# Kernel optimization log

Measured on AMD Instinct MI355X. Metric: run time of the kernel, lower is better.

The kernel has to match this reference:

```python
import jax, jax.numpy as jnp
import numpy as np

B, C, H, W = 8, 256, 64, 64
IC = 64  # inter_channels


def conv1x1(x, w, b):
    # x: [B,C,H,W], w: [O,C], b: [O]
    return jnp.einsum('bchw,oc->bohw', x, w) + b[None, :, None, None]


def maxpool2(x):
    # 2x2 max pool, stride 2. x: [B,C,H,W]
    b, c, h, w = x.shape
    return x.reshape(b, c, h // 2, 2, w // 2, 2).max(axis=(3, 5))


def setup_inputs() -> dict:
    key = jax.random.key(0)
    ks = jax.random.split(key, 9)
    s_in = 1.0 / np.sqrt(C)
    s_ic = 1.0 / np.sqrt(IC)
    return {
        'x': jax.random.normal(ks[0], (B, C, H, W), dtype=jnp.float32),
        'g_w': jax.random.uniform(ks[1], (IC, C), jnp.float32, -s_in, s_in),
        'g_b': jax.random.uniform(ks[2], (IC,), jnp.float32, -s_in, s_in),
        'theta_w': jax.random.uniform(ks[3], (IC, C), jnp.float32, -s_in, s_in),
        'theta_b': jax.random.uniform(ks[4], (IC,), jnp.float32, -s_in, s_in),
        'phi_w': jax.random.uniform(ks[5], (IC, C), jnp.float32, -s_in, s_in),
        'phi_b': jax.random.uniform(ks[6], (IC,), jnp.float32, -s_in, s_in),
        'W_w': jax.random.uniform(ks[7], (C, IC), jnp.float32, -np.sqrt(6.0 / IC), np.sqrt(6.0 / IC)),
        'W_b': jax.random.uniform(ks[8], (C,), jnp.float32, -s_ic, s_ic),
    }


def reference(x, g_w, g_b, theta_w, theta_b, phi_w, phi_b, W_w, W_b):
    b, c, h, w = x.shape
    n = h * w                     # query positions
    m = (h // 2) * (w // 2)       # pooled key/value positions

    v = maxpool2(conv1x1(x, g_w, g_b)).reshape(b, IC, m).transpose(0, 2, 1)   # [b,m,ic]
    q = conv1x1(x, theta_w, theta_b).reshape(b, IC, n).transpose(0, 2, 1)     # [b,n,ic]
    k = maxpool2(conv1x1(x, phi_w, phi_b)).reshape(b, IC, m)                  # [b,ic,m]

    attn = jax.nn.softmax(jnp.einsum('bni,bim->bnm', q, k), axis=-1)          # [b,n,m]
    attended = jnp.einsum('bnm,bmi->bni', attn, v)                            # [b,n,ic]
    attended = attended.transpose(0, 2, 1).reshape(b, IC, h, w)
    # F.interpolate to (h,w) is identity here: attended already has spatial (h,w)
    return conv1x1(attended, W_w, W_b) + x
```

## Files before the change

kernel.cpp:

```cpp
#include <hip/hip_runtime.h>

typedef unsigned short ushort_t;
typedef unsigned int   uint_t;

typedef __attribute__((ext_vector_type(8))) short  short8;
typedef __attribute__((ext_vector_type(4))) short  short4v;
typedef __attribute__((ext_vector_type(4))) float  float4v;

#define BB    8
#define CC    256
#define HH    64
#define WW2   64
#define NPIX  4096
#define MPOS  1024
#define ICH   64

__device__ __forceinline__ float bf2f(ushort_t u) {
  return __uint_as_float(((uint_t)u) << 16);
}
__device__ __forceinline__ ushort_t f2bf(float f) {
  uint_t i = __float_as_uint(f);
  uint_t r = (i + 0x7FFFu + ((i >> 16) & 1u)) >> 16;
  return (ushort_t)r;
}
__device__ __forceinline__ ushort_t f2bf_rna(float f) {
  return (ushort_t)((__float_as_uint(f) + 0x8000u) >> 16);
}
__device__ __forceinline__ uint_t pack2(float a, float b) {
  return (uint_t)f2bf(a) | ((uint_t)f2bf(b) << 16);
}

__device__ __forceinline__ void gl2lds16(const ushort_t* g, ushort_t* l) {
  __builtin_amdgcn_global_load_lds(
      (const __attribute__((address_space(1))) void*)g,
      (__attribute__((address_space(3))) void*)l, 16, 0, 0);
}

__global__ __launch_bounds__(256) void prep_kernel(
    const float* __restrict__ theta_w, const float* __restrict__ phi_w,
    const float* __restrict__ g_w, const float* __restrict__ W_w,
    const float* __restrict__ theta_b, const float* __restrict__ phi_b,
    const float* __restrict__ g_b,
    ushort_t* __restrict__ wA2, ushort_t* __restrict__ Wbf2,
    float* __restrict__ biasAll) {
  int i = blockIdx.x * 256 + threadIdx.x;
  if (i < 49152) {
    float v = (i < 16384) ? theta_w[i]
            : (i < 32768) ? phi_w[i - 16384]
                          : g_w[i - 32768];
    int o = i >> 8, c = i & 255;
    wA2[(c >> 3) * 1536 + o * 8 + (c & 7)] = f2bf(v);
  } else if (i < 65536) {
    int j = i - 49152;
    int o = j >> 6, ic = j & 63;
    Wbf2[(ic >> 3) * 2048 + o * 8 + (ic & 7)] = f2bf(W_w[j]);
  } else if (i < 65600)    biasAll[i - 65536] = theta_b[i - 65536];
  else if (i < 65664)      biasAll[i - 65536] = phi_b[i - 65600];
  else if (i < 65728)      biasAll[i - 65536] = g_b[i - 65664];
}

__global__ __launch_bounds__(256, 2) void qkv_kernel(
    const float* __restrict__ x, const ushort_t* __restrict__ wA2,
    const float* __restrict__ biasAll,
    ushort_t* __restrict__ qbuf, ushort_t* __restrict__ kTbuf,
    ushort_t* __restrict__ vTbuf) {
  __shared__ __align__(16) ushort_t Bsu[64 * 256];
  uint4* Bs16 = (uint4*)Bsu;
  int tid = threadIdx.x;
  int wave = tid >> 6, lane = tid & 63;
  int quad = lane >> 4, col = lane & 15;
  int b = blockIdx.x & 7, t = blockIdx.x >> 3;
  int rj = t >> 1, h = t & 1;

  {
    int pg = tid & 15, cb = tid >> 4;
    int prow = pg >> 3;
    int pcol = (pg * 4) & 31;
    const float* xsrc = x + (size_t)b * (CC * NPIX) +
                        (size_t)(2 * rj + prow) * WW2 + h * 32 + pcol;
    float4 v[16];
#pragma unroll
    for (int c = 0; c < 16; ++c)
      v[c] = *(const float4*)&xsrc[(size_t)(cb * 16 + c) * NPIX];
#pragma unroll
    for (int j = 0; j < 4; ++j) {
      int pos = pg * 4 + j;
      uint4 w0, w1;
      w0.x = pack2(v[0][j],  v[1][j]);
      w0.y = pack2(v[2][j],  v[3][j]);
      w0.z = pack2(v[4][j],  v[5][j]);
      w0.w = pack2(v[6][j],  v[7][j]);
      w1.x = pack2(v[8][j],  v[9][j]);
      w1.y = pack2(v[10][j], v[11][j]);
      w1.z = pack2(v[12][j], v[13][j]);
      w1.w = pack2(v[14][j], v[15][j]);
      int jb0 = cb * 2, jb1 = cb * 2 + 1;
      Bs16[pos * 32 + (jb0 & ~7) + ((jb0 & 7) ^ (pos & 7))] = w0;
      Bs16[pos * 32 + (jb1 & ~7) + ((jb1 & 7) ^ (pos & 7))] = w1;
    }
  }
  __syncthreads();

  float4v acc[3][4];
#pragma unroll
  for (int ot = 0; ot < 3; ++ot) {
    int ob = wave * 48 + ot * 16 + quad * 4;
    float4v bv;
#pragma unroll
    for (int r = 0; r < 4; ++r) bv[r] = biasAll[ob + r];
#pragma unroll
    for (int s = 0; s < 4; ++s) acc[ot][s] = bv;
  }

  const uint4* wA16 = (const uint4*)wA2;
#pragma unroll
  for (int ks = 0; ks < 8; ++ks) {
    int kblk = ks * 4 + quad;
    short8 aw[3];
#pragma unroll
    for (int ot = 0; ot < 3; ++ot) {
      uint4 a = wA16[kblk * 192 + wave * 48 + ot * 16 + col];
      aw[ot] = *(const short8*)&a;
    }
#pragma unroll
    for (int s = 0; s < 4; ++s) {
      int lp = s * 16 + col;
      uint4 braw = Bs16[lp * 32 + (kblk & ~7) + ((kblk & 7) ^ (lp & 7))];
      short8 bx = *(const short8*)&braw;
#pragma unroll
      for (int ot = 0; ot < 3; ++ot)
        acc[ot][s] = __builtin_amdgcn_mfma_f32_16x16x32_bf16(aw[ot], bx, acc[ot][s], 0, 0, 0);
    }
  }

#pragma unroll
  for (int ot = 0; ot < 3; ++ot) {
    int ob = wave * 48 + ot * 16;
    if (ob < 64) {
#pragma unroll
      for (int s = 0; s < 4; ++s) {
        int n = (2 * rj + (s >> 1)) * WW2 + h * 32 + (s & 1) * 16 + col;
        uint2 u;
        u.x = pack2(acc[ot][s][0], acc[ot][s][1]);
        u.y = pack2(acc[ot][s][2], acc[ot][s][3]);
        *(uint2*)&qbuf[((size_t)(b * NPIX + n)) * ICH + ob + quad * 4] = u;
      }
    } else if (ob < 128) {
#pragma unroll
      for (int s = 0; s < 2; ++s) {
        float4v pm;
#pragma unroll
        for (int r = 0; r < 4; ++r) {
          float v = fmaxf(acc[ot][s][r], acc[ot][s + 2][r]);
          pm[r] = fmaxf(v, __shfl_xor(v, 1));
        }
        if ((lane & 1) == 0) {
          int m = rj * 32 + h * 16 + s * 8 + (col >> 1);
          uint2 u;
          u.x = pack2(pm[0], pm[1]);
          u.y = pack2(pm[2], pm[3]);
          *(uint2*)&kTbuf[((size_t)(b * MPOS + m)) * ICH + (ob - 64) + quad * 4] = u;
        }
      }
    } else {
#pragma unroll
      for (int s = 0; s < 2; ++s) {
        float4v pm;
#pragma unroll
        for (int r = 0; r < 4; ++r) {
          float v = fmaxf(acc[ot][s][r], acc[ot][s + 2][r]);
          pm[r] = fmaxf(v, __shfl_xor(v, 1));
        }
        if ((lane & 1) == 0) {
          int m = rj * 32 + h * 16 + s * 8 + (col >> 1);
#pragma unroll
          for (int r = 0; r < 4; ++r)
            vTbuf[((size_t)(b * ICH + (ob - 128) + quad * 4 + r)) * MPOS + m] = f2bf(pm[r]);
        }
      }
    }
  }
}

__global__ __launch_bounds__(256, 2) void attn_out_kernel(
    const ushort_t* __restrict__ qbuf, const ushort_t* __restrict__ kTbuf,
    const ushort_t* __restrict__ vTbuf, const ushort_t* __restrict__ Wbf2,
    const float* __restrict__ W_b, const float* __restrict__ x,
    float* __restrict__ out) {
  __shared__ __align__(16) ushort_t Ks[2][64 * 64];
  __shared__ __align__(16) ushort_t Vs[2][64 * 64];
  __shared__ __align__(16) ushort_t Ps[4][16 * 72];
  int tid  = threadIdx.x;
  int wave = tid >> 6, lane = tid & 63;
  int quad = lane >> 4, col = lane & 15;
  int b = blockIdx.x & 7, qt = blockIdx.x >> 3;

  ushort_t* Psw = &Ps[wave][0];

  const ushort_t* qrow = qbuf + ((size_t)(b * NPIX + qt * 64 + wave * 16 + col)) * ICH;
  short8 aQ0 = *(const short8*)&qrow[quad * 8];
  short8 aQ1 = *(const short8*)&qrow[32 + quad * 8];

  int srow = tid >> 3, sblk = tid & 7;
  int swz  = (sblk ^ (srow & 7)) * 8;
  const ushort_t* kg = kTbuf + (size_t)b * MPOS * ICH;
  const ushort_t* vg = vTbuf + (size_t)b * ICH * MPOS;
  const ushort_t* kg0 = kg + srow * ICH + swz;
  const ushort_t* kg1 = kg + (32 + srow) * ICH + swz;
  const ushort_t* vg0 = vg + (size_t)srow * MPOS + swz;
  const ushort_t* vg1 = vg + (size_t)(32 + srow) * MPOS + swz;

#define STAGE(bufi, kt)                                          \
  do {                                                           \
    gl2lds16(kg0 + (kt) * 4096, &Ks[bufi][wave * 512]);          \
    gl2lds16(kg1 + (kt) * 4096, &Ks[bufi][2048 + wave * 512]);   \
    gl2lds16(vg0 + (kt) * 64,   &Vs[bufi][wave * 512]);          \
    gl2lds16(vg1 + (kt) * 64,   &Vs[bufi][2048 + wave * 512]);   \
  } while (0)

  STAGE(0, 0);
  __syncthreads();

  const float4v zero4 = {0.f, 0.f, 0.f, 0.f};
  float l_lane = 0.f;
  float4v o_acc[4];
#pragma unroll
  for (int t = 0; t < 4; ++t) o_acc[t] = zero4;

  for (int kt = 0; kt < 16; ++kt) {
    int buf = kt & 1;
    if (kt < 15) STAGE(buf ^ 1, kt + 1);

    float4v s_acc[4];
    __builtin_amdgcn_s_setprio(1);
#pragma unroll
    for (int t = 0; t < 4; ++t) {
      float4v s = zero4;
      short8 ak0 = *(const short8*)&Ks[buf][(t * 16 + col) * 64 + ((quad ^ (col & 7)) * 8)];
      s = __builtin_amdgcn_mfma_f32_16x16x32_bf16(ak0, aQ0, s, 0, 0, 0);
      short8 ak1 = *(const short8*)&Ks[buf][(t * 16 + col) * 64 + (((4 + quad) ^ (col & 7)) * 8)];
      s = __builtin_amdgcn_mfma_f32_16x16x32_bf16(ak1, aQ1, s, 0, 0, 0);
      s_acc[t] = s;
    }
    __builtin_amdgcn_s_setprio(0);

#pragma unroll
    for (int t = 0; t < 4; ++t) {
      float p0 = __expf(s_acc[t][0]);
      float p1 = __expf(s_acc[t][1]);
      float p2 = __expf(s_acc[t][2]);
      float p3 = __expf(s_acc[t][3]);
      l_lane += (p0 + p1) + (p2 + p3);
      uint2 u;
      u.x = (uint_t)f2bf_rna(p0) | ((uint_t)f2bf_rna(p1) << 16);
      u.y = (uint_t)f2bf_rna(p2) | ((uint_t)f2bf_rna(p3) << 16);
      *(uint2*)&Psw[col * 72 + t * 16 + quad * 4] = u;
    }

    __builtin_amdgcn_s_setprio(1);
#pragma unroll
    for (int kk = 0; kk < 2; ++kk) {
      short8 ap = *(const short8*)&Psw[col * 72 + kk * 32 + quad * 8];
#pragma unroll
      for (int t = 0; t < 4; ++t) {
        short8 bv = *(const short8*)&Vs[buf][(t * 16 + col) * 64 + (((kk * 4 + quad) ^ (col & 7)) * 8)];
        o_acc[t] = __builtin_amdgcn_mfma_f32_16x16x32_bf16(ap, bv, o_acc[t], 0, 0, 0);
      }
    }
    __builtin_amdgcn_s_setprio(0);

    __syncthreads();
  }
#undef STAGE

  l_lane += __shfl_xor(l_lane, 16);
  l_lane += __shfl_xor(l_lane, 32);
  float invl = 1.0f / l_lane;

#pragma unroll
  for (int r = 0; r < 4; ++r) {
    float iv = __shfl(invl, (lane & 48) | (quad * 4 + r));
    int prow = (quad * 4 + r) * 72;
#pragma unroll
    for (int t = 0; t < 4; ++t)
      Psw[prow + t * 16 + col] = f2bf(o_acc[t][r] * iv);
  }

  short8 ap0 = *(const short8*)&Psw[col * 72 + quad * 8];
  short8 ap1 = *(const short8*)&Psw[col * 72 + 32 + quad * 8];
  const uint4* W16 = (const uint4*)Wbf2;
  int pbase = qt * 64 + wave * 16 + quad * 4;
#pragma unroll
  for (int ot = 0; ot < 16; ++ot) {
    float bvv = W_b[ot * 16 + col];
    float4v c = {bvv, bvv, bvv, bvv};
    uint4 w0 = W16[quad * 256 + ot * 16 + col];
    uint4 w1 = W16[(4 + quad) * 256 + ot * 16 + col];
    c = __builtin_amdgcn_mfma_f32_16x16x32_bf16(ap0, *(const short8*)&w0, c, 0, 0, 0);
    c = __builtin_amdgcn_mfma_f32_16x16x32_bf16(ap1, *(const short8*)&w1, c, 0, 0, 0);
    size_t idx = ((size_t)(b * CC + ot * 16 + col)) * NPIX + pbase;
    float4 xv = *(const float4*)&x[idx];
    float4 ov;
    ov.x = c[0] + xv.x;
    ov.y = c[1] + xv.y;
    ov.z = c[2] + xv.z;
    ov.w = c[3] + xv.w;
    *(float4*)&out[idx] = ov;
  }
}

extern "C" void kernel_launch(void* const* d_in, const int* in_sizes, int n_in,
                              void* d_out, int out_size, void* d_ws, size_t ws_size,
                              hipStream_t stream) {
  const float* x       = (const float*)d_in[0];
  const float* g_w     = (const float*)d_in[1];
  const float* g_b     = (const float*)d_in[2];
  const float* theta_w = (const float*)d_in[3];
  const float* theta_b = (const float*)d_in[4];
  const float* phi_w   = (const float*)d_in[5];
  const float* phi_b   = (const float*)d_in[6];
  const float* W_w     = (const float*)d_in[7];
  const float* W_b     = (const float*)d_in[8];
  (void)in_sizes; (void)n_in; (void)out_size; (void)ws_size;

  char* ws = (char*)d_ws;
  ushort_t* wA2     = (ushort_t*)(ws + 0);
  ushort_t* Wbf2    = (ushort_t*)(ws + 98304);
  float*    biasAll = (float*)(ws + 131072);
  ushort_t* qbuf    = (ushort_t*)(ws + 262144);
  ushort_t* kTbuf   = (ushort_t*)(ws + 4456448);
  ushort_t* vTbuf   = (ushort_t*)(ws + 5505024);
  float* out = (float*)d_out;

  prep_kernel<<<257, 256, 0, stream>>>(theta_w, phi_w, g_w, W_w,
                                       theta_b, phi_b, g_b,
                                       wA2, Wbf2, biasAll);
  qkv_kernel<<<512, 256, 0, stream>>>(x, wA2, biasAll, qbuf, kTbuf, vTbuf);
  attn_out_kernel<<<512, 256, 0, stream>>>(qbuf, kTbuf, vTbuf, Wbf2, W_b, x, out);
}
```

Baseline: 131.3 us.

## Fuse QKV projection and attention kernels with a software grid barrier

```diff
diff --git a/kernel.cpp b/kernel.cpp
--- a/kernel.cpp
+++ b/kernel.cpp
@@ -4,7 +4,6 @@
 typedef unsigned int   uint_t;
 
 typedef __attribute__((ext_vector_type(8))) short  short8;
-typedef __attribute__((ext_vector_type(4))) short  short4v;
 typedef __attribute__((ext_vector_type(4))) float  float4v;
 
 #define BB    8
@@ -14,10 +13,8 @@
 #define NPIX  4096
 #define MPOS  1024
 #define ICH   64
-
-__device__ __forceinline__ float bf2f(ushort_t u) {
-  return __uint_as_float(((uint_t)u) << 16);
-}
+#define NBLK  512
+
 __device__ __forceinline__ ushort_t f2bf(float f) {
   uint_t i = __float_as_uint(f);
   uint_t r = (i + 0x7FFFu + ((i >> 16) & 1u)) >> 16;
@@ -34,6 +31,21 @@
   __builtin_amdgcn_global_load_lds(
       (const __attribute__((address_space(1))) void*)g,
       (__attribute__((address_space(3))) void*)l, 16, 0, 0);
+}
+
+__device__ __forceinline__ void grid_barrier(uint_t* bar) {
+  __syncthreads();
+  if (threadIdx.x == 0) {
+    __threadfence();
+    atomicAdd(bar, 1u);
+    int guard = 0;
+    while (atomicAdd(bar, 0u) < NBLK && guard < (1 << 20)) {
+      __builtin_amdgcn_s_sleep(8);
+      ++guard;
+    }
+    __threadfence();
+  }
+  __syncthreads();
 }
 
 __global__ __launch_bounds__(256) void prep_kernel(
@@ -59,253 +71,254 @@
   else if (i < 65728)      biasAll[i - 65536] = g_b[i - 65664];
 }
 
-__global__ __launch_bounds__(256, 2) void qkv_kernel(
+__global__ __launch_bounds__(256, 2) void fused_qkv_attn(
     const float* __restrict__ x, const ushort_t* __restrict__ wA2,
-    const float* __restrict__ biasAll,
+    const float* __restrict__ biasAll, const ushort_t* __restrict__ Wbf2,
+    const float* __restrict__ W_b,
     ushort_t* __restrict__ qbuf, ushort_t* __restrict__ kTbuf,
-    ushort_t* __restrict__ vTbuf) {
-  __shared__ __align__(16) ushort_t Bsu[64 * 256];
-  uint4* Bs16 = (uint4*)Bsu;
+    ushort_t* __restrict__ vTbuf, uint_t* __restrict__ bar,
+    float* __restrict__ out) {
+  __shared__ __align__(16) ushort_t SH[20992];
   int tid = threadIdx.x;
   int wave = tid >> 6, lane = tid & 63;
   int quad = lane >> 4, col = lane & 15;
-  int b = blockIdx.x & 7, t = blockIdx.x >> 3;
-  int rj = t >> 1, h = t & 1;
+  int b = blockIdx.x & 7;
 
   {
-    int pg = tid & 15, cb = tid >> 4;
-    int prow = pg >> 3;
-    int pcol = (pg * 4) & 31;
-    const float* xsrc = x + (size_t)b * (CC * NPIX) +
-                        (size_t)(2 * rj + prow) * WW2 + h * 32 + pcol;
-    float4 v[16];
-#pragma unroll
-    for (int c = 0; c < 16; ++c)
-      v[c] = *(const float4*)&xsrc[(size_t)(cb * 16 + c) * NPIX];
-#pragma unroll
-    for (int j = 0; j < 4; ++j) {
-      int pos = pg * 4 + j;
-      uint4 w0, w1;
-      w0.x = pack2(v[0][j],  v[1][j]);
-      w0.y = pack2(v[2][j],  v[3][j]);
-      w0.z = pack2(v[4][j],  v[5][j]);
-      w0.w = pack2(v[6][j],  v[7][j]);
-      w1.x = pack2(v[8][j],  v[9][j]);
-      w1.y = pack2(v[10][j], v[11][j]);
-      w1.z = pack2(v[12][j], v[13][j]);
-      w1.w = pack2(v[14][j], v[15][j]);
-      int jb0 = cb * 2, jb1 = cb * 2 + 1;
-      Bs16[pos * 32 + (jb0 & ~7) + ((jb0 & 7) ^ (pos & 7))] = w0;
-      Bs16[pos * 32 + (jb1 & ~7) + ((jb1 & 7) ^ (pos & 7))] = w1;
+    uint4* Bs16 = (uint4*)SH;
+    int t = blockIdx.x >> 3;
+    int rj = t >> 1, h = t & 1;
+
+    {
+      int pg = tid & 15, cb = tid >> 4;
+      int prow = pg >> 3;
+      int pcol = (pg * 4) & 31;
+      const float* xsrc = x + (size_t)b * (CC * NPIX) +
+                          (size_t)(2 * rj + prow) * WW2 + h * 32 + pcol;
+      float4 v[16];
+#pragma unroll
+      for (int c = 0; c < 16; ++c)
+        v[c] = *(const float4*)&xsrc[(size_t)(cb * 16 + c) * NPIX];
+#pragma unroll
+      for (int j = 0; j < 4; ++j) {
+        int pos = pg * 4 + j;
+        uint4 w0, w1;
+        w0.x = pack2(v[0][j],  v[1][j]);
+        w0.y = pack2(v[2][j],  v[3][j]);
+        w0.z = pack2(v[4][j],  v[5][j]);
+        w0.w = pack2(v[6][j],  v[7][j]);
+        w1.x = pack2(v[8][j],  v[9][j]);
+        w1.y = pack2(v[10][j], v[11][j]);
+        w1.z = pack2(v[12][j], v[13][j]);
+        w1.w = pack2(v[14][j], v[15][j]);
+        int jb0 = cb * 2, jb1 = cb * 2 + 1;
+        Bs16[pos * 32 + (jb0 & ~7) + ((jb0 & 7) ^ (pos & 7))] = w0;
+        Bs16[pos * 32 + (jb1 & ~7) + ((jb1 & 7) ^ (pos & 7))] = w1;
+      }
+    }
+    __syncthreads();
+
+    float4v acc[3][4];
+#pragma unroll
+    for (int ot = 0; ot < 3; ++ot) {
+      int ob = wave * 48 + ot * 16 + quad * 4;
+      float4v bv;
+#pragma unroll
+      for (int r = 0; r < 4; ++r) bv[r] = biasAll[ob + r];
+#pragma unroll
+      for (int s = 0; s < 4; ++s) acc[ot][s] = bv;
+    }
+
+    const uint4* wA16 = (const uint4*)wA2;
+#pragma unroll
+    for (int ks = 0; ks < 8; ++ks) {
+      int kblk = ks * 4 + quad;
+      short8 aw[3];
+#pragma unroll
+      for (int ot = 0; ot < 3; ++ot) {
+        uint4 a = wA16[kblk * 192 + wave * 48 + ot * 16 + col];
+        aw[ot] = *(const short8*)&a;
+      }
+#pragma unroll
+      for (int s = 0; s < 4; ++s) {
+        int lp = s * 16 + col;
+        uint4 braw = Bs16[lp * 32 + (kblk & ~7) + ((kblk & 7) ^ (lp & 7))];
+        short8 bx = *(const short8*)&braw;
+#pragma unroll
+        for (int ot = 0; ot < 3; ++ot)
+          acc[ot][s] = __builtin_amdgcn_mfma_f32_16x16x32_bf16(aw[ot], bx, acc[ot][s], 0, 0, 0);
+      }
+    }
+
+#pragma unroll
+    for (int ot = 0; ot < 3; ++ot) {
+      int ob = wave * 48 + ot * 16;
+      if (ob < 64) {
+#pragma unroll
+        for (int s = 0; s < 4; ++s) {
+          int n = (2 * rj + (s >> 1)) * WW2 + h * 32 + (s & 1) * 16 + col;
+          uint2 u;
+          u.x = pack2(acc[ot][s][0], acc[ot][s][1]);
+          u.y = pack2(acc[ot][s][2], acc[ot][s][3]);
+          *(uint2*)&qbuf[((size_t)(b * NPIX + n)) * ICH + ob + quad * 4] = u;
+        }
+      } else if (ob < 128) {
+#pragma unroll
+        for (int s = 0; s < 2; ++s) {
+          float4v pm;
+#pragma unroll
+          for (int r = 0; r < 4; ++r) {
+            float v = fmaxf(acc[ot][s][r], acc[ot][s + 2][r]);
+            pm[r] = fmaxf(v, __shfl_xor(v, 1));
+          }
+          if ((lane & 1) == 0) {
+            int m = rj * 32 + h * 16 + s * 8 + (col >> 1);
+            uint2 u;
+            u.x = pack2(pm[0], pm[1]);
+            u.y = pack2(pm[2], pm[3]);
+            *(uint2*)&kTbuf[((size_t)(b * MPOS + m)) * ICH + (ob - 64) + quad * 4] = u;
+          }
+        }
+      } else {
+#pragma unroll
+        for (int s = 0; s < 2; ++s) {
+          float4v pm;
+#pragma unroll
+          for (int r = 0; r < 4; ++r) {
+            float v = fmaxf(acc[ot][s][r], acc[ot][s + 2][r]);
+            pm[r] = fmaxf(v, __shfl_xor(v, 1));
+          }
+          if ((lane & 1) == 0) {
+            int m = rj * 32 + h * 16 + s * 8 + (col >> 1);
+#pragma unroll
+            for (int r = 0; r < 4; ++r)
+              vTbuf[((size_t)(b * ICH + (ob - 128) + quad * 4 + r)) * MPOS + m] = f2bf(pm[r]);
+          }
+        }
+      }
     }
   }
-  __syncthreads();
-
-  float4v acc[3][4];
-#pragma unroll
-  for (int ot = 0; ot < 3; ++ot) {
-    int ob = wave * 48 + ot * 16 + quad * 4;
-    float4v bv;
-#pragma unroll
-    for (int r = 0; r < 4; ++r) bv[r] = biasAll[ob + r];
-#pragma unroll
-    for (int s = 0; s < 4; ++s) acc[ot][s] = bv;
-  }
-
-  const uint4* wA16 = (const uint4*)wA2;
-#pragma unroll
-  for (int ks = 0; ks < 8; ++ks) {
-    int kblk = ks * 4 + quad;
-    short8 aw[3];
-#pragma unroll
-    for (int ot = 0; ot < 3; ++ot) {
-      uint4 a = wA16[kblk * 192 + wave * 48 + ot * 16 + col];
-      aw[ot] = *(const short8*)&a;
-    }
-#pragma unroll
-    for (int s = 0; s < 4; ++s) {
-      int lp = s * 16 + col;
-      uint4 braw = Bs16[lp * 32 + (kblk & ~7) + ((kblk & 7) ^ (lp & 7))];
-      short8 bx = *(const short8*)&braw;
-#pragma unroll
-      for (int ot = 0; ot < 3; ++ot)
-        acc[ot][s] = __builtin_amdgcn_mfma_f32_16x16x32_bf16(aw[ot], bx, acc[ot][s], 0, 0, 0);
-    }
-  }
-
-#pragma unroll
-  for (int ot = 0; ot < 3; ++ot) {
-    int ob = wave * 48 + ot * 16;
-    if (ob < 64) {
-#pragma unroll
-      for (int s = 0; s < 4; ++s) {
-        int n = (2 * rj + (s >> 1)) * WW2 + h * 32 + (s & 1) * 16 + col;
+
+  grid_barrier(bar);
+
+  {
+    ushort_t* Ks0 = SH;
+    ushort_t* Vs0 = SH + 8192;
+    ushort_t* Ps  = SH + 16384;
+    int qt = blockIdx.x >> 3;
+
+    ushort_t* Psw = Ps + wave * (16 * 72);
+
+    const ushort_t* qrow = qbuf + ((size_t)(b * NPIX + qt * 64 + wave * 16 + col)) * ICH;
+    short8 aQ0 = *(const short8*)&qrow[quad * 8];
+    short8 aQ1 = *(const short8*)&qrow[32 + quad * 8];
+
+    int srow = tid >> 3, sblk = tid & 7;
+    int swz  = (sblk ^ (srow & 7)) * 8;
+    const ushort_t* kg = kTbuf + (size_t)b * MPOS * ICH;
+    const ushort_t* vg = vTbuf + (size_t)b * ICH * MPOS;
+    const ushort_t* kg0 = kg + srow * ICH + swz;
+    const ushort_t* kg1 = kg + (32 + srow) * ICH + swz;
+    const ushort_t* vg0 = vg + (size_t)srow * MPOS + swz;
+    const ushort_t* vg1 = vg + (size_t)(32 + srow) * MPOS + swz;
+
+#define STAGE(bufi, kt)                                               \
+    do {                                                              \
+      gl2lds16(kg0 + (kt) * 4096, Ks0 + (bufi) * 4096 + wave * 512);  \
+      gl2lds16(kg1 + (kt) * 4096, Ks0 + (bufi) * 4096 + 2048 + wave * 512); \
+      gl2lds16(vg0 + (kt) * 64,   Vs0 + (bufi) * 4096 + wave * 512);  \
+      gl2lds16(vg1 + (kt) * 64,   Vs0 + (bufi) * 4096 + 2048 + wave * 512); \
+    } while (0)
+
+    STAGE(0, 0);
+    __syncthreads();
+
+    const float4v zero4 = {0.f, 0.f, 0.f, 0.f};
+    float l_lane = 0.f;
+    float4v o_acc[4];
+#pragma unroll
+    for (int t = 0; t < 4; ++t) o_acc[t] = zero4;
+
+    for (int kt = 0; kt < 16; ++kt) {
+      int buf = kt & 1;
+      if (kt < 15) STAGE(buf ^ 1, kt + 1);
+
+      float4v s_acc[4];
+      __builtin_amdgcn_s_setprio(1);
+#pragma unroll
+      for (int t = 0; t < 4; ++t) {
+        float4v s = zero4;
+        short8 ak0 = *(const short8*)&Ks0[buf * 4096 + (t * 16 + col) * 64 + ((quad ^ (col & 7)) * 8)];
+        s = __builtin_amdgcn_mfma_f32_16x16x32_bf16(ak0, aQ0, s, 0, 0, 0);
+        short8 ak1 = *(const short8*)&Ks0[buf * 4096 + (t * 16 + col) * 64 + (((4 + quad) ^ (col & 7)) * 8)];
+        s = __builtin_amdgcn_mfma_f32_16x16x32_bf16(ak1, aQ1, s, 0, 0, 0);
+        s_acc[t] = s;
+      }
+      __builtin_amdgcn_s_setprio(0);
+
+#pragma unroll
+      for (int t = 0; t < 4; ++t) {
+        float p0 = __expf(s_acc[t][0]);
+        float p1 = __expf(s_acc[t][1]);
+        float p2 = __expf(s_acc[t][2]);
+        float p3 = __expf(s_acc[t][3]);
+        l_lane += (p0 + p1) + (p2 + p3);
         uint2 u;
-        u.x = pack2(acc[ot][s][0], acc[ot][s][1]);
-        u.y = pack2(acc[ot][s][2], acc[ot][s][3]);
-        *(uint2*)&qbuf[((size_t)(b * NPIX + n)) * ICH + ob + quad * 4] = u;
-      }
-    } else if (ob < 128) {
-#pragma unroll
-      for (int s = 0; s < 2; ++s) {
-        float4v pm;
-#pragma unroll
-        for (int r = 0; r < 4; ++r) {
-          float v = fmaxf(acc[ot][s][r], acc[ot][s + 2][r]);
-          pm[r] = fmaxf(v, __shfl_xor(v, 1));
+        u.x = (uint_t)f2bf_rna(p0) | ((uint_t)f2bf_rna(p1) << 16);
+        u.y = (uint_t)f2bf_rna(p2) | ((uint_t)f2bf_rna(p3) << 16);
+        *(uint2*)&Psw[col * 72 + t * 16 + quad * 4] = u;
+      }
+
+      __builtin_amdgcn_s_setprio(1);
+#pragma unroll
+      for (int kk = 0; kk < 2; ++kk) {
+        short8 ap = *(const short8*)&Psw[col * 72 + kk * 32 + quad * 8];
+#pragma unroll
+        for (int t = 0; t < 4; ++t) {
+          short8 bv = *(const short8*)&Vs0[buf * 4096 + (t * 16 + col) * 64 + (((kk * 4 + quad) ^ (col & 7)) * 8)];
+          o_acc[t] = __builtin_amdgcn_mfma_f32_16x16x32_bf16(ap, bv, o_acc[t], 0, 0, 0);
         }
-        if ((lane & 1) == 0) {
-          int m = rj * 32 + h * 16 + s * 8 + (col >> 1);
-          uint2 u;
-          u.x = pack2(pm[0], pm[1]);
-          u.y = pack2(pm[2], pm[3]);
-          *(uint2*)&kTbuf[((size_t)(b * MPOS + m)) * ICH + (ob - 64) + quad * 4] = u;
-        }
-      }
-    } else {
-#pragma unroll
-      for (int s = 0; s < 2; ++s) {
-        float4v pm;
-#pragma unroll
-        for (int r = 0; r < 4; ++r) {
-          float v = fmaxf(acc[ot][s][r], acc[ot][s + 2][r]);
-          pm[r] = fmaxf(v, __shfl_xor(v, 1));
-        }
-        if ((lane & 1) == 0) {
-          int m = rj * 32 + h * 16 + s * 8 + (col >> 1);
-#pragma unroll
-          for (int r = 0; r < 4; ++r)
-            vTbuf[((size_t)(b * ICH + (ob - 128) + quad * 4 + r)) * MPOS + m] = f2bf(pm[r]);
-        }
-      }
-    }
-  }
-}
-
-__global__ __launch_bounds__(256, 2) void attn_out_kernel(
-    const ushort_t* __restrict__ qbuf, const ushort_t* __restrict__ kTbuf,
-    const ushort_t* __restrict__ vTbuf, const ushort_t* __restrict__ Wbf2,
-    const float* __restrict__ W_b, const float* __restrict__ x,
-    float* __restrict__ out) {
-  __shared__ __align__(16) ushort_t Ks[2][64 * 64];
-  __shared__ __align__(16) ushort_t Vs[2][64 * 64];
-  __shared__ __align__(16) ushort_t Ps[4][16 * 72];
-  int tid  = threadIdx.x;
-  int wave = tid >> 6, lane = tid & 63;
-  int quad = lane >> 4, col = lane & 15;
-  int b = blockIdx.x & 7, qt = blockIdx.x >> 3;
-
-  ushort_t* Psw = &Ps[wave][0];
-
-  const ushort_t* qrow = qbuf + ((size_t)(b * NPIX + qt * 64 + wave * 16 + col)) * ICH;
-  short8 aQ0 = *(const short8*)&qrow[quad * 8];
-  short8 aQ1 = *(const short8*)&qrow[32 + quad * 8];
-
-  int srow = tid >> 3, sblk = tid & 7;
-  int swz  = (sblk ^ (srow & 7)) * 8;
-  const ushort_t* kg = kTbuf + (size_t)b * MPOS * ICH;
-  const ushort_t* vg = vTbuf + (size_t)b * ICH * MPOS;
-  const ushort_t* kg0 = kg + srow * ICH + swz;
-  const ushort_t* kg1 = kg + (32 + srow) * ICH + swz;
-  const ushort_t* vg0 = vg + (size_t)srow * MPOS + swz;
-  const ushort_t* vg1 = vg + (size_t)(32 + srow) * MPOS + swz;
-
-#define STAGE(bufi, kt)                                          \
-  do {                                                           \
-    gl2lds16(kg0 + (kt) * 4096, &Ks[bufi][wave * 512]);          \
-    gl2lds16(kg1 + (kt) * 4096, &Ks[bufi][2048 + wave * 512]);   \
-    gl2lds16(vg0 + (kt) * 64,   &Vs[bufi][wave * 512]);          \
-    gl2lds16(vg1 + (kt) * 64,   &Vs[bufi][2048 + wave * 512]);   \
-  } while (0)
-
-  STAGE(0, 0);
-  __syncthreads();
-
-  const float4v zero4 = {0.f, 0.f, 0.f, 0.f};
-  float l_lane = 0.f;
-  float4v o_acc[4];
-#pragma unroll
-  for (int t = 0; t < 4; ++t) o_acc[t] = zero4;
-
-  for (int kt = 0; kt < 16; ++kt) {
-    int buf = kt & 1;
-    if (kt < 15) STAGE(buf ^ 1, kt + 1);
-
-    float4v s_acc[4];
-    __builtin_amdgcn_s_setprio(1);
-#pragma unroll
-    for (int t = 0; t < 4; ++t) {
-      float4v s = zero4;
-      short8 ak0 = *(const short8*)&Ks[buf][(t * 16 + col) * 64 + ((quad ^ (col & 7)) * 8)];
-      s = __builtin_amdgcn_mfma_f32_16x16x32_bf16(ak0, aQ0, s, 0, 0, 0);
-      short8 ak1 = *(const short8*)&Ks[buf][(t * 16 + col) * 64 + (((4 + quad) ^ (col & 7)) * 8)];
-      s = __builtin_amdgcn_mfma_f32_16x16x32_bf16(ak1, aQ1, s, 0, 0, 0);
-      s_acc[t] = s;
-    }
-    __builtin_amdgcn_s_setprio(0);
-
-#pragma unroll
-    for (int t = 0; t < 4; ++t) {
-      float p0 = __expf(s_acc[t][0]);
-      float p1 = __expf(s_acc[t][1]);
-      float p2 = __expf(s_acc[t][2]);
-      float p3 = __expf(s_acc[t][3]);
-      l_lane += (p0 + p1) + (p2 + p3);
-      uint2 u;
-      u.x = (uint_t)f2bf_rna(p0) | ((uint_t)f2bf_rna(p1) << 16);
-      u.y = (uint_t)f2bf_rna(p2) | ((uint_t)f2bf_rna(p3) << 16);
-      *(uint2*)&Psw[col * 72 + t * 16 + quad * 4] = u;
-    }
-
-    __builtin_amdgcn_s_setprio(1);
-#pragma unroll
-    for (int kk = 0; kk < 2; ++kk) {
-      short8 ap = *(const short8*)&Psw[col * 72 + kk * 32 + quad * 8];
-#pragma unroll
-      for (int t = 0; t < 4; ++t) {
-        short8 bv = *(const short8*)&Vs[buf][(t * 16 + col) * 64 + (((kk * 4 + quad) ^ (col & 7)) * 8)];
-        o_acc[t] = __builtin_amdgcn_mfma_f32_16x16x32_bf16(ap, bv, o_acc[t], 0, 0, 0);
-      }
-    }
-    __builtin_amdgcn_s_setprio(0);
-
-    __syncthreads();
-  }
+      }
+      __builtin_amdgcn_s_setprio(0);
+
+      __syncthreads();
+    }
 #undef STAGE
 
-  l_lane += __shfl_xor(l_lane, 16);
-  l_lane += __shfl_xor(l_lane, 32);
-  float invl = 1.0f / l_lane;
-
-#pragma unroll
-  for (int r = 0; r < 4; ++r) {
-    float iv = __shfl(invl, (lane & 48) | (quad * 4 + r));
-    int prow = (quad * 4 + r) * 72;
-#pragma unroll
-    for (int t = 0; t < 4; ++t)
-      Psw[prow + t * 16 + col] = f2bf(o_acc[t][r] * iv);
-  }
-
-  short8 ap0 = *(const short8*)&Psw[col * 72 + quad * 8];
-  short8 ap1 = *(const short8*)&Psw[col * 72 + 32 + quad * 8];
-  const uint4* W16 = (const uint4*)Wbf2;
-  int pbase = qt * 64 + wave * 16 + quad * 4;
-#pragma unroll
-  for (int ot = 0; ot < 16; ++ot) {
-    float bvv = W_b[ot * 16 + col];
-    float4v c = {bvv, bvv, bvv, bvv};
-    uint4 w0 = W16[quad * 256 + ot * 16 + col];
-    uint4 w1 = W16[(4 + quad) * 256 + ot * 16 + col];
-    c = __builtin_amdgcn_mfma_f32_16x16x32_bf16(ap0, *(const short8*)&w0, c, 0, 0, 0);
-    c = __builtin_amdgcn_mfma_f32_16x16x32_bf16(ap1, *(const short8*)&w1, c, 0, 0, 0);
-    size_t idx = ((size_t)(b * CC + ot * 16 + col)) * NPIX + pbase;
-    float4 xv = *(const float4*)&x[idx];
-    float4 ov;
-    ov.x = c[0] + xv.x;
-    ov.y = c[1] + xv.y;
-    ov.z = c[2] + xv.z;
-    ov.w = c[3] + xv.w;
-    *(float4*)&out[idx] = ov;
+    l_lane += __shfl_xor(l_lane, 16);
+    l_lane += __shfl_xor(l_lane, 32);
+    float invl = 1.0f / l_lane;
+
+#pragma unroll
+    for (int r = 0; r < 4; ++r) {
+      float iv = __shfl(invl, (lane & 48) | (quad * 4 + r));
+      int prow = (quad * 4 + r) * 72;
+#pragma unroll
+      for (int t = 0; t < 4; ++t)
+        Psw[prow + t * 16 + col] = f2bf(o_acc[t][r] * iv);
+    }
+
+    short8 ap0 = *(const short8*)&Psw[col * 72 + quad * 8];
+    short8 ap1 = *(const short8*)&Psw[col * 72 + 32 + quad * 8];
+    const uint4* W16 = (const uint4*)Wbf2;
+    int pbase = qt * 64 + wave * 16 + quad * 4;
+#pragma unroll
+    for (int ot = 0; ot < 16; ++ot) {
+      float bvv = W_b[ot * 16 + col];
+      float4v c = {bvv, bvv, bvv, bvv};
+      uint4 w0 = W16[quad * 256 + ot * 16 + col];
+      uint4 w1 = W16[(4 + quad) * 256 + ot * 16 + col];
+      c = __builtin_amdgcn_mfma_f32_16x16x32_bf16(ap0, *(const short8*)&w0, c, 0, 0, 0);
+      c = __builtin_amdgcn_mfma_f32_16x16x32_bf16(ap1, *(const short8*)&w1, c, 0, 0, 0);
+      size_t idx = ((size_t)(b * CC + ot * 16 + col)) * NPIX + pbase;
+      float4 xv = *(const float4*)&x[idx];
+      float4 ov;
+      ov.x = c[0] + xv.x;
+      ov.y = c[1] + xv.y;
+      ov.z = c[2] + xv.z;
+      ov.w = c[3] + xv.w;
+      *(float4*)&out[idx] = ov;
+    }
   }
 }
 
@@ -327,14 +340,16 @@
   ushort_t* wA2     = (ushort_t*)(ws + 0);
   ushort_t* Wbf2    = (ushort_t*)(ws + 98304);
   float*    biasAll = (float*)(ws + 131072);
+  uint_t*   bar     = (uint_t*)(ws + 196608);
   ushort_t* qbuf    = (ushort_t*)(ws + 262144);
   ushort_t* kTbuf   = (ushort_t*)(ws + 4456448);
   ushort_t* vTbuf   = (ushort_t*)(ws + 5505024);
   float* out = (float*)d_out;
 
+  hipMemsetAsync(bar, 0, 256, stream);
   prep_kernel<<<257, 256, 0, stream>>>(theta_w, phi_w, g_w, W_w,
                                        theta_b, phi_b, g_b,
                                        wA2, Wbf2, biasAll);
-  qkv_kernel<<<512, 256, 0, stream>>>(x, wA2, biasAll, qbuf, kTbuf, vTbuf);
-  attn_out_kernel<<<512, 256, 0, stream>>>(qbuf, kTbuf, vTbuf, Wbf2, W_b, x, out);
-}
+  fused_qkv_attn<<<512, 256, 0, stream>>>(x, wA2, biasAll, Wbf2, W_b,
+                                          qbuf, kTbuf, vTbuf, bar, out);
+}
```

Measured after the change: 180.4 us. 1.37x slower.

## Enlarge attention tiles to 128 queries and 256-key chunks, single-buffered

Applied to the files above, without the earlier changes.

```diff
diff --git a/kernel.cpp b/kernel.cpp
--- a/kernel.cpp
+++ b/kernel.cpp
@@ -4,7 +4,6 @@
 typedef unsigned int   uint_t;
 
 typedef __attribute__((ext_vector_type(8))) short  short8;
-typedef __attribute__((ext_vector_type(4))) short  short4v;
 typedef __attribute__((ext_vector_type(4))) float  float4v;
 
 #define BB    8
@@ -15,9 +14,6 @@
 #define MPOS  1024
 #define ICH   64
 
-__device__ __forceinline__ float bf2f(ushort_t u) {
-  return __uint_as_float(((uint_t)u) << 16);
-}
 __device__ __forceinline__ ushort_t f2bf(float f) {
   uint_t i = __float_as_uint(f);
   uint_t r = (i + 0x7FFFu + ((i >> 16) & 1u)) >> 16;
@@ -182,43 +178,50 @@
   }
 }
 
-__global__ __launch_bounds__(256, 2) void attn_out_kernel(
+__global__ __launch_bounds__(512) void attn_out_kernel(
     const ushort_t* __restrict__ qbuf, const ushort_t* __restrict__ kTbuf,
     const ushort_t* __restrict__ vTbuf, const ushort_t* __restrict__ Wbf2,
     const float* __restrict__ W_b, const float* __restrict__ x,
     float* __restrict__ out) {
-  __shared__ __align__(16) ushort_t Ks[2][64 * 64];
-  __shared__ __align__(16) ushort_t Vs[2][64 * 64];
-  __shared__ __align__(16) ushort_t Ps[4][16 * 72];
+  extern __shared__ __align__(16) ushort_t SH[];
+  ushort_t* Ks = SH;
+  ushort_t* Vs = SH + 16384;
+  ushort_t* Ps = SH + 32768;
   int tid  = threadIdx.x;
   int wave = tid >> 6, lane = tid & 63;
   int quad = lane >> 4, col = lane & 15;
   int b = blockIdx.x & 7, qt = blockIdx.x >> 3;
 
-  ushort_t* Psw = &Ps[wave][0];
-
-  const ushort_t* qrow = qbuf + ((size_t)(b * NPIX + qt * 64 + wave * 16 + col)) * ICH;
+  ushort_t* Psw = Ps + wave * (16 * 40);
+
+  const ushort_t* qrow = qbuf + ((size_t)(b * NPIX + qt * 128 + wave * 16 + col)) * ICH;
   short8 aQ0 = *(const short8*)&qrow[quad * 8];
   short8 aQ1 = *(const short8*)&qrow[32 + quad * 8];
 
-  int srow = tid >> 3, sblk = tid & 7;
-  int swz  = (sblk ^ (srow & 7)) * 8;
-  const ushort_t* kg = kTbuf + (size_t)b * MPOS * ICH;
-  const ushort_t* vg = vTbuf + (size_t)b * ICH * MPOS;
-  const ushort_t* kg0 = kg + srow * ICH + swz;
-  const ushort_t* kg1 = kg + (32 + srow) * ICH + swz;
-  const ushort_t* vg0 = vg + (size_t)srow * MPOS + swz;
-  const ushort_t* vg1 = vg + (size_t)(32 + srow) * MPOS + swz;
-
-#define STAGE(bufi, kt)                                          \
-  do {                                                           \
-    gl2lds16(kg0 + (kt) * 4096, &Ks[bufi][wave * 512]);          \
-    gl2lds16(kg1 + (kt) * 4096, &Ks[bufi][2048 + wave * 512]);   \
-    gl2lds16(vg0 + (kt) * 64,   &Vs[bufi][wave * 512]);          \
-    gl2lds16(vg1 + (kt) * 64,   &Vs[bufi][2048 + wave * 512]);   \
+  int srow8 = lane >> 3, sblk = lane & 7;
+  const ushort_t* kgL = kTbuf + (size_t)b * MPOS * ICH +
+                        (wave * 8 + srow8) * ICH + ((sblk ^ srow8) * 8);
+  const ushort_t* vgL[4];
+  int vblk = lane & 31;
+#pragma unroll
+  for (int g = 0; g < 4; ++g) {
+    int vic = wave * 8 + g * 2 + (lane >> 5);
+    int swz = ((vblk & ~7) | ((vblk & 7) ^ (vic & 7))) * 8;
+    vgL[g] = vTbuf + (size_t)b * ICH * MPOS + (size_t)vic * MPOS + swz;
+  }
+
+#define STAGE(kt)                                                         \
+  do {                                                                    \
+    _Pragma("unroll")                                                     \
+    for (int g = 0; g < 4; ++g)                                           \
+      gl2lds16(kgL + ((kt) * 256 + g * 64) * ICH,                         \
+               Ks + (g * 64 + wave * 8) * 64);                            \
+    _Pragma("unroll")                                                     \
+    for (int g = 0; g < 4; ++g)                                           \
+      gl2lds16(vgL[g] + (kt) * 256, Vs + (wave * 8 + g * 2) * 256);       \
   } while (0)
 
-  STAGE(0, 0);
+  STAGE(0);
   __syncthreads();
 
   const float4v zero4 = {0.f, 0.f, 0.f, 0.f};
@@ -227,49 +230,44 @@
 #pragma unroll
   for (int t = 0; t < 4; ++t) o_acc[t] = zero4;
 
-  for (int kt = 0; kt < 16; ++kt) {
-    int buf = kt & 1;
-    if (kt < 15) STAGE(buf ^ 1, kt + 1);
-
-    float4v s_acc[4];
-    __builtin_amdgcn_s_setprio(1);
-#pragma unroll
-    for (int t = 0; t < 4; ++t) {
-      float4v s = zero4;
-      short8 ak0 = *(const short8*)&Ks[buf][(t * 16 + col) * 64 + ((quad ^ (col & 7)) * 8)];
-      s = __builtin_amdgcn_mfma_f32_16x16x32_bf16(ak0, aQ0, s, 0, 0, 0);
-      short8 ak1 = *(const short8*)&Ks[buf][(t * 16 + col) * 64 + (((4 + quad) ^ (col & 7)) * 8)];
-      s = __builtin_amdgcn_mfma_f32_16x16x32_bf16(ak1, aQ1, s, 0, 0, 0);
-      s_acc[t] = s;
-    }
-    __builtin_amdgcn_s_setprio(0);
-
-#pragma unroll
-    for (int t = 0; t < 4; ++t) {
-      float p0 = __expf(s_acc[t][0]);
-      float p1 = __expf(s_acc[t][1]);
-      float p2 = __expf(s_acc[t][2]);
-      float p3 = __expf(s_acc[t][3]);
-      l_lane += (p0 + p1) + (p2 + p3);
-      uint2 u;
-      u.x = (uint_t)f2bf_rna(p0) | ((uint_t)f2bf_rna(p1) << 16);
-      u.y = (uint_t)f2bf_rna(p2) | ((uint_t)f2bf_rna(p3) << 16);
-      *(uint2*)&Psw[col * 72 + t * 16 + quad * 4] = u;
-    }
-
-    __builtin_amdgcn_s_setprio(1);
-#pragma unroll
-    for (int kk = 0; kk < 2; ++kk) {
-      short8 ap = *(const short8*)&Psw[col * 72 + kk * 32 + quad * 8];
+  int kswz0 = (quad ^ (col & 7)) * 8;
+  int kswz1 = ((4 + quad) ^ (col & 7)) * 8;
+
+  for (int it = 0; it < 4; ++it) {
+#pragma unroll
+    for (int c = 0; c < 8; ++c) {
+#pragma unroll
+      for (int hh = 0; hh < 2; ++hh) {
+        int tt = c * 2 + hh;
+        float4v s = zero4;
+        short8 ak0 = *(const short8*)&Ks[(tt * 16 + col) * 64 + kswz0];
+        s = __builtin_amdgcn_mfma_f32_16x16x32_bf16(ak0, aQ0, s, 0, 0, 0);
+        short8 ak1 = *(const short8*)&Ks[(tt * 16 + col) * 64 + kswz1];
+        s = __builtin_amdgcn_mfma_f32_16x16x32_bf16(ak1, aQ1, s, 0, 0, 0);
+        float p0 = __expf(s[0]);
+        float p1 = __expf(s[1]);
+        float p2 = __expf(s[2]);
+        float p3 = __expf(s[3]);
+        l_lane += (p0 + p1) + (p2 + p3);
+        uint2 u;
+        u.x = (uint_t)f2bf_rna(p0) | ((uint_t)f2bf_rna(p1) << 16);
+        u.y = (uint_t)f2bf_rna(p2) | ((uint_t)f2bf_rna(p3) << 16);
+        *(uint2*)&Psw[col * 40 + hh * 16 + quad * 4] = u;
+      }
+      short8 ap = *(const short8*)&Psw[col * 40 + quad * 8];
+      int blk = c * 4 + quad;
 #pragma unroll
       for (int t = 0; t < 4; ++t) {
-        short8 bv = *(const short8*)&Vs[buf][(t * 16 + col) * 64 + (((kk * 4 + quad) ^ (col & 7)) * 8)];
+        int rswz = ((blk & ~7) | ((blk & 7) ^ (col & 7))) * 8;
+        short8 bv = *(const short8*)&Vs[(t * 16 + col) * 256 + rswz];
         o_acc[t] = __builtin_amdgcn_mfma_f32_16x16x32_bf16(ap, bv, o_acc[t], 0, 0, 0);
       }
     }
-    __builtin_amdgcn_s_setprio(0);
-
     __syncthreads();
+    if (it < 3) {
+      STAGE(it + 1);
+      __syncthreads();
+    }
   }
 #undef STAGE
 
@@ -277,19 +275,20 @@
   l_lane += __shfl_xor(l_lane, 32);
   float invl = 1.0f / l_lane;
 
+  ushort_t* Att = Ks + wave * (16 * 72);
 #pragma unroll
   for (int r = 0; r < 4; ++r) {
     float iv = __shfl(invl, (lane & 48) | (quad * 4 + r));
     int prow = (quad * 4 + r) * 72;
 #pragma unroll
     for (int t = 0; t < 4; ++t)
-      Psw[prow + t * 16 + col] = f2bf(o_acc[t][r] * iv);
-  }
-
-  short8 ap0 = *(const short8*)&Psw[col * 72 + quad * 8];
-  short8 ap1 = *(const short8*)&Psw[col * 72 + 32 + quad * 8];
+      Att[prow + t * 16 + col] = f2bf(o_acc[t][r] * iv);
+  }
+
+  short8 ap0 = *(const short8*)&Att[col * 72 + quad * 8];
+  short8 ap1 = *(const short8*)&Att[col * 72 + 32 + quad * 8];
   const uint4* W16 = (const uint4*)Wbf2;
-  int pbase = qt * 64 + wave * 16 + quad * 4;
+  int pbase = qt * 128 + wave * 16 + quad * 4;
 #pragma unroll
   for (int ot = 0; ot < 16; ++ot) {
     float bvv = W_b[ot * 16 + col];
@@ -332,9 +331,17 @@
   ushort_t* vTbuf   = (ushort_t*)(ws + 5505024);
   float* out = (float*)d_out;
 
+  static bool attr_done = false;
+  if (!attr_done) {
+    hipFuncSetAttribute((const void*)attn_out_kernel,
+                        hipFuncAttributeMaxDynamicSharedMemorySize, 75776);
+    attr_done = true;
+  }
+
   prep_kernel<<<257, 256, 0, stream>>>(theta_w, phi_w, g_w, W_w,
                                        theta_b, phi_b, g_b,
                                        wA2, Wbf2, biasAll);
   qkv_kernel<<<512, 256, 0, stream>>>(x, wA2, biasAll, qbuf, kTbuf, vTbuf);
-  attn_out_kernel<<<512, 256, 0, stream>>>(qbuf, kTbuf, vTbuf, Wbf2, W_b, x, out);
-}
+  attn_out_kernel<<<256, 512, 75776, stream>>>(qbuf, kTbuf, vTbuf, Wbf2,
+                                               W_b, x, out);
+}
```

After: 127.4 us. -3.0%, faster.
